# Performance work log

Measured on AMD Instinct MI355X. Metric: run time of the kernel, lower is better.

Reference implementation:

```python
import jax, jax.numpy as jnp
import numpy as np


def _dct_1d(x):
    # cat(x, flip(x)) -> fft(norm='forward') -> first L bins -> |.| * sign(Re)
    L = x.shape[-1]
    arr = jnp.concatenate([x, jnp.flip(x, axis=-1)], axis=-1)  # [..., 2L]
    f = jnp.fft.fft(arr, norm='forward')[..., :L]
    return jnp.abs(f) * jnp.sign(f.real)


def _dct_2d(x):
    row = _dct_1d(x)
    col = _dct_1d(row.swapaxes(-1, -2))
    return col.swapaxes(-1, -2)


def setup_inputs() -> dict:
    key = jax.random.key(0)
    k1, k2, k3 = jax.random.split(key, 3)
    B, C, H, W = 16, 256, 64, 64
    r = 16
    ip = jax.random.normal(k1, (B, C, H, W), dtype=jnp.float32)
    w1 = jax.random.normal(k2, (C, C // r), dtype=jnp.float32) * (1.0 / np.sqrt(C))
    w2 = jax.random.normal(k3, (C // r, C), dtype=jnp.float32) * (1.0 / np.sqrt(C // r))
    return {"ip": ip, "w1": w1, "w2": w2}


def reference(ip, w1, w2):
    B, C, H, W = ip.shape
    dct = _dct_2d(ip)                                  # [B,C,H,W]
    top1 = jnp.max(dct.reshape(B, C, H * W), axis=-1)  # top-k(k=1) == max, [B,C]
    h = jax.nn.relu(top1 @ w1)                         # [B, C//r]
    weights = jax.nn.sigmoid(h @ w2)                   # [B, C]
    return ip * weights[:, :, None, None]
```

## Files before the change

kernel.cpp:

```cpp
#include <hip/hip_runtime.h>
#include <math.h>


#define S 72

typedef __attribute__((ext_vector_type(8))) short bf16x8;
typedef __attribute__((ext_vector_type(4))) float f32x4;

__device__ inline unsigned short f2bf(float x) {
    union { float f; unsigned u; } v; v.f = x;
    unsigned r = v.u + 0x7FFF + ((v.u >> 16) & 1);
    return (unsigned short)(r >> 16);
}

__global__ __launch_bounds__(256, 4) void dct_max_kernel(const float* __restrict__ ip,
                                                         float* __restrict__ top1) {
    __shared__ unsigned short Dbf[64 * S];
    __shared__ unsigned short Xbf[64 * S];
    __shared__ unsigned short Tbf[64 * S];
    __shared__ float red[4];

    const int t = threadIdx.x;

#pragma unroll
    for (int i = 0; i < 16; ++i) {
        int idx = i * 256 + t;
        int u = idx >> 6, h = idx & 63;
        int mm = (u * (2 * h + 1)) & 255;
        Dbf[u * S + h] = f2bf(cospif((float)mm * (1.0f / 128.0f)));
    }

    const int wv = t >> 6;
    const int l = t & 63;
    const int m = l & 15;
    const int q = l >> 4;
    const int arow = (16 * wv + m) * S + 8 * q;
    const int xh = t >> 4;
    const int xw0 = (4 * t) & 63;

    const int bc0 = blockIdx.x * 4;
    const float4* src4 = (const float4*)(ip + (size_t)bc0 * 4096);

    float4 xv[4];
#pragma unroll
    for (int i = 0; i < 4; ++i) xv[i] = src4[i * 256 + t];

    __syncthreads();
    const bf16x8 da0 = *(const bf16x8*)&Dbf[arow];
    const bf16x8 da1 = *(const bf16x8*)&Dbf[arow + 32];

    for (int s = 0; s < 4; ++s) {
#pragma unroll
        for (int i = 0; i < 4; ++i) {
            ushort4 p;
            p.x = f2bf(xv[i].x); p.y = f2bf(xv[i].y);
            p.z = f2bf(xv[i].z); p.w = f2bf(xv[i].w);
            *(ushort4*)&Xbf[(16 * i + xh) * S + xw0] = p;
        }
        __syncthreads();

        if (s < 3) {
            const float4* nsrc = src4 + (size_t)(s + 1) * 1024;
#pragma unroll
            for (int i = 0; i < 4; ++i) xv[i] = nsrc[i * 256 + t];
        }

        f32x4 acc[4];
#pragma unroll
        for (int tn = 0; tn < 4; ++tn) {
            const int brow = (16 * tn + m) * S + 8 * q;
            bf16x8 b0 = *(const bf16x8*)&Xbf[brow];
            bf16x8 b1 = *(const bf16x8*)&Xbf[brow + 32];
            f32x4 c = {0.0f, 0.0f, 0.0f, 0.0f};
            c = __builtin_amdgcn_mfma_f32_16x16x32_bf16(da0, b0, c, 0, 0, 0);
            c = __builtin_amdgcn_mfma_f32_16x16x32_bf16(da1, b1, c, 0, 0, 0);
            acc[tn] = c;
        }
#pragma unroll
        for (int tn = 0; tn < 4; ++tn)
#pragma unroll
            for (int reg = 0; reg < 4; ++reg)
                Tbf[(16 * wv + 4 * q + reg) * S + 16 * tn + m] = f2bf(acc[tn][reg]);
        __syncthreads();

        bf16x8 ta0 = *(const bf16x8*)&Tbf[arow];
        bf16x8 ta1 = *(const bf16x8*)&Tbf[arow + 32];
        float mx = -3.4e38f;
#pragma unroll
        for (int tn = 0; tn < 4; ++tn) {
            const int brow = (16 * tn + m) * S + 8 * q;
            bf16x8 b0 = *(const bf16x8*)&Dbf[brow];
            bf16x8 b1 = *(const bf16x8*)&Dbf[brow + 32];
            f32x4 c = {0.0f, 0.0f, 0.0f, 0.0f};
            c = __builtin_amdgcn_mfma_f32_16x16x32_bf16(ta0, b0, c, 0, 0, 0);
            c = __builtin_amdgcn_mfma_f32_16x16x32_bf16(ta1, b1, c, 0, 0, 0);
            mx = fmaxf(mx, fmaxf(fmaxf(c[0], c[1]), fmaxf(c[2], c[3])));
        }

#pragma unroll
        for (int off = 32; off > 0; off >>= 1) mx = fmaxf(mx, __shfl_down(mx, off, 64));
        if (l == 0) red[wv] = mx;
        __syncthreads();
        if (t == 0) {
            float M = fmaxf(fmaxf(red[0], red[1]), fmaxf(red[2], red[3]));
            top1[bc0 + s] = M * (1.0f / 4096.0f);
        }
    }
}

__global__ __launch_bounds__(256, 4) void scale_kernel(const float* __restrict__ ip,
                                                       const float* __restrict__ top1,
                                                       const float* __restrict__ w1,
                                                       const float* __restrict__ w2,
                                                       float* __restrict__ out) {
    __shared__ float h_s[16];
    __shared__ float w_s[4];
    const int t = threadIdx.x;
    const int bc0 = blockIdx.x * 4;
    const int b = bc0 >> 8, c0 = bc0 & 255;

    const f32x4* ip4 = (const f32x4*)ip + (size_t)bc0 * 1024;
    f32x4* out4 = (f32x4*)out + (size_t)bc0 * 1024;

    const int j = t >> 4, i = t & 15;
    float tvals[16], wvals[16];
#pragma unroll
    for (int k = 0; k < 16; ++k) {
        int cc = i + 16 * k;
        tvals[k] = top1[b * 256 + cc];
        wvals[k] = w1[cc * 16 + j];
    }
    f32x4 v[16];
#pragma unroll
    for (int s = 0; s < 4; ++s)
#pragma unroll
        for (int k = 0; k < 4; ++k) v[s * 4 + k] = ip4[(size_t)s * 1024 + k * 256 + t];

    float partial = 0.0f;
#pragma unroll
    for (int k = 0; k < 16; ++k) partial = fmaf(tvals[k], wvals[k], partial);
#pragma unroll
    for (int off = 8; off > 0; off >>= 1) partial += __shfl_xor(partial, off, 16);
    if (i == 0) h_s[j] = fmaxf(partial, 0.0f);
    __syncthreads();

    if (t < 64) {
        const int sc = t >> 4, jj = t & 15;
        float p2 = h_s[jj] * w2[jj * 256 + (c0 + sc)];
#pragma unroll
        for (int off = 8; off > 0; off >>= 1) p2 += __shfl_xor(p2, off, 16);
        if (jj == 0) w_s[sc] = 1.0f / (1.0f + __expf(-p2));
    }
    __syncthreads();

#pragma unroll
    for (int s = 0; s < 4; ++s) {
        const float wt = w_s[s];
#pragma unroll
        for (int k = 0; k < 4; ++k) {
            f32x4 r = v[s * 4 + k] * wt;
            __builtin_nontemporal_store(r, &out4[(size_t)s * 1024 + k * 256 + t]);
        }
    }
}

extern "C" void kernel_launch(void* const* d_in, const int* in_sizes, int n_in,
                              void* d_out, int out_size, void* d_ws, size_t ws_size,
                              hipStream_t stream) {
    const float* ip = (const float*)d_in[0];
    const float* w1 = (const float*)d_in[1];
    const float* w2 = (const float*)d_in[2];
    float* out = (float*)d_out;
    float* top1 = (float*)d_ws;

    dct_max_kernel<<<1024, 256, 0, stream>>>(ip, top1);
    scale_kernel<<<1024, 256, 0, stream>>>(ip, top1, w1, w2, out);
}
```

Measured before the change: 127.1 us.

## Process one channel per block and use packed bf16 conversion instructions

Both kernels now handle one (batch, channel) plane per block instead of four, so the grid grows from 1024 to 4096 blocks and the per-block loop with register prefetch of the next plane goes away. The scale kernel keeps only four vectors in registers instead of sixteen, which lowers register pressure. Float-to-bf16 conversion now uses the hardware v_cvt_pk_bf16_f32 instruction instead of manual rounding. In exchange, each block rebuilds the DCT basis table in shared memory and recomputes the small MLP four times as often, and the software prefetch overlap is lost.

```diff
diff --git a/kernel.cpp b/kernel.cpp
--- a/kernel.cpp
+++ b/kernel.cpp
@@ -6,6 +6,12 @@
 
 typedef __attribute__((ext_vector_type(8))) short bf16x8;
 typedef __attribute__((ext_vector_type(4))) float f32x4;
+
+__device__ inline unsigned cvt_pk_bf16(float lo, float hi) {
+    unsigned r;
+    asm("v_cvt_pk_bf16_f32 %0, %1, %2" : "=v"(r) : "v"(lo), "v"(hi));
+    return r;
+}
 
 __device__ inline unsigned short f2bf(float x) {
     union { float f; unsigned u; } v; v.f = x;
@@ -21,6 +27,12 @@
     __shared__ float red[4];
 
     const int t = threadIdx.x;
+    const int bc = blockIdx.x;
+
+    const float4* src4 = (const float4*)(ip + (size_t)bc * 4096);
+    float4 xv[4];
+#pragma unroll
+    for (int i = 0; i < 4; ++i) xv[i] = src4[i * 256 + t];
 
 #pragma unroll
     for (int i = 0; i < 16; ++i) {
@@ -38,73 +50,58 @@
     const int xh = t >> 4;
     const int xw0 = (4 * t) & 63;
 
-    const int bc0 = blockIdx.x * 4;
-    const float4* src4 = (const float4*)(ip + (size_t)bc0 * 4096);
+#pragma unroll
+    for (int i = 0; i < 4; ++i) {
+        uint2 p;
+        p.x = cvt_pk_bf16(xv[i].x, xv[i].y);
+        p.y = cvt_pk_bf16(xv[i].z, xv[i].w);
+        *(uint2*)&Xbf[(16 * i + xh) * S + xw0] = p;
+    }
+    __syncthreads();
 
-    float4 xv[4];
-#pragma unroll
-    for (int i = 0; i < 4; ++i) xv[i] = src4[i * 256 + t];
-
-    __syncthreads();
     const bf16x8 da0 = *(const bf16x8*)&Dbf[arow];
     const bf16x8 da1 = *(const bf16x8*)&Dbf[arow + 32];
 
-    for (int s = 0; s < 4; ++s) {
+    f32x4 acc[4];
 #pragma unroll
-        for (int i = 0; i < 4; ++i) {
-            ushort4 p;
-            p.x = f2bf(xv[i].x); p.y = f2bf(xv[i].y);
-            p.z = f2bf(xv[i].z); p.w = f2bf(xv[i].w);
-            *(ushort4*)&Xbf[(16 * i + xh) * S + xw0] = p;
-        }
-        __syncthreads();
+    for (int tn = 0; tn < 4; ++tn) {
+        const int brow = (16 * tn + m) * S + 8 * q;
+        bf16x8 b0 = *(const bf16x8*)&Xbf[brow];
+        bf16x8 b1 = *(const bf16x8*)&Xbf[brow + 32];
+        f32x4 c = {0.0f, 0.0f, 0.0f, 0.0f};
+        c = __builtin_amdgcn_mfma_f32_16x16x32_bf16(da0, b0, c, 0, 0, 0);
+        c = __builtin_amdgcn_mfma_f32_16x16x32_bf16(da1, b1, c, 0, 0, 0);
+        acc[tn] = c;
+    }
+#pragma unroll
+    for (int tn = 0; tn < 4; ++tn)
+#pragma unroll
+        for (int reg = 0; reg < 4; ++reg)
+            Tbf[(16 * wv + 4 * q + reg) * S + 16 * tn + m] =
+                (unsigned short)cvt_pk_bf16(acc[tn][reg], acc[tn][reg]);
+    __syncthreads();
 
-        if (s < 3) {
-            const float4* nsrc = src4 + (size_t)(s + 1) * 1024;
+    bf16x8 ta0 = *(const bf16x8*)&Tbf[arow];
+    bf16x8 ta1 = *(const bf16x8*)&Tbf[arow + 32];
+    float mx = -3.4e38f;
 #pragma unroll
-            for (int i = 0; i < 4; ++i) xv[i] = nsrc[i * 256 + t];
-        }
-
-        f32x4 acc[4];
-#pragma unroll
-        for (int tn = 0; tn < 4; ++tn) {
-            const int brow = (16 * tn + m) * S + 8 * q;
-            bf16x8 b0 = *(const bf16x8*)&Xbf[brow];
-            bf16x8 b1 = *(const bf16x8*)&Xbf[brow + 32];
-            f32x4 c = {0.0f, 0.0f, 0.0f, 0.0f};
-            c = __builtin_amdgcn_mfma_f32_16x16x32_bf16(da0, b0, c, 0, 0, 0);
-            c = __builtin_amdgcn_mfma_f32_16x16x32_bf16(da1, b1, c, 0, 0, 0);
-            acc[tn] = c;
-        }
-#pragma unroll
-        for (int tn = 0; tn < 4; ++tn)
-#pragma unroll
-            for (int reg = 0; reg < 4; ++reg)
-                Tbf[(16 * wv + 4 * q + reg) * S + 16 * tn + m] = f2bf(acc[tn][reg]);
-        __syncthreads();
-
-        bf16x8 ta0 = *(const bf16x8*)&Tbf[arow];
-        bf16x8 ta1 = *(const bf16x8*)&Tbf[arow + 32];
-        float mx = -3.4e38f;
-#pragma unroll
-        for (int tn = 0; tn < 4; ++tn) {
-            const int brow = (16 * tn + m) * S + 8 * q;
-            bf16x8 b0 = *(const bf16x8*)&Dbf[brow];
-            bf16x8 b1 = *(const bf16x8*)&Dbf[brow + 32];
-            f32x4 c = {0.0f, 0.0f, 0.0f, 0.0f};
-            c = __builtin_amdgcn_mfma_f32_16x16x32_bf16(ta0, b0, c, 0, 0, 0);
-            c = __builtin_amdgcn_mfma_f32_16x16x32_bf16(ta1, b1, c, 0, 0, 0);
-            mx = fmaxf(mx, fmaxf(fmaxf(c[0], c[1]), fmaxf(c[2], c[3])));
-        }
+    for (int tn = 0; tn < 4; ++tn) {
+        const int brow = (16 * tn + m) * S + 8 * q;
+        bf16x8 b0 = *(const bf16x8*)&Dbf[brow];
+        bf16x8 b1 = *(const bf16x8*)&Dbf[brow + 32];
+        f32x4 c = {0.0f, 0.0f, 0.0f, 0.0f};
+        c = __builtin_amdgcn_mfma_f32_16x16x32_bf16(ta0, b0, c, 0, 0, 0);
+        c = __builtin_amdgcn_mfma_f32_16x16x32_bf16(ta1, b1, c, 0, 0, 0);
+        mx = fmaxf(mx, fmaxf(fmaxf(c[0], c[1]), fmaxf(c[2], c[3])));
+    }
 
 #pragma unroll
-        for (int off = 32; off > 0; off >>= 1) mx = fmaxf(mx, __shfl_down(mx, off, 64));
-        if (l == 0) red[wv] = mx;
-        __syncthreads();
-        if (t == 0) {
-            float M = fmaxf(fmaxf(red[0], red[1]), fmaxf(red[2], red[3]));
-            top1[bc0 + s] = M * (1.0f / 4096.0f);
-        }
+    for (int off = 32; off > 0; off >>= 1) mx = fmaxf(mx, __shfl_down(mx, off, 64));
+    if (l == 0) red[wv] = mx;
+    __syncthreads();
+    if (t == 0) {
+        float M = fmaxf(fmaxf(red[0], red[1]), fmaxf(red[2], red[3]));
+        top1[bc] = M * (1.0f / 4096.0f);
     }
 }
 
@@ -114,54 +111,42 @@
                                                        const float* __restrict__ w2,
                                                        float* __restrict__ out) {
     __shared__ float h_s[16];
-    __shared__ float w_s[4];
+    __shared__ float wsc;
     const int t = threadIdx.x;
-    const int bc0 = blockIdx.x * 4;
-    const int b = bc0 >> 8, c0 = bc0 & 255;
+    const int bc = blockIdx.x;
+    const int b = bc >> 8, c = bc & 255;
 
-    const f32x4* ip4 = (const f32x4*)ip + (size_t)bc0 * 1024;
-    f32x4* out4 = (f32x4*)out + (size_t)bc0 * 1024;
+    const f32x4* ip4 = (const f32x4*)ip + (size_t)bc * 1024;
+    f32x4* out4 = (f32x4*)out + (size_t)bc * 1024;
+
+    f32x4 v[4];
+#pragma unroll
+    for (int k = 0; k < 4; ++k) v[k] = ip4[k * 256 + t];
 
     const int j = t >> 4, i = t & 15;
-    float tvals[16], wvals[16];
+    float partial = 0.0f;
 #pragma unroll
     for (int k = 0; k < 16; ++k) {
         int cc = i + 16 * k;
-        tvals[k] = top1[b * 256 + cc];
-        wvals[k] = w1[cc * 16 + j];
+        partial = fmaf(top1[b * 256 + cc], w1[cc * 16 + j], partial);
     }
-    f32x4 v[16];
-#pragma unroll
-    for (int s = 0; s < 4; ++s)
-#pragma unroll
-        for (int k = 0; k < 4; ++k) v[s * 4 + k] = ip4[(size_t)s * 1024 + k * 256 + t];
-
-    float partial = 0.0f;
-#pragma unroll
-    for (int k = 0; k < 16; ++k) partial = fmaf(tvals[k], wvals[k], partial);
 #pragma unroll
     for (int off = 8; off > 0; off >>= 1) partial += __shfl_xor(partial, off, 16);
     if (i == 0) h_s[j] = fmaxf(partial, 0.0f);
     __syncthreads();
 
-    if (t < 64) {
-        const int sc = t >> 4, jj = t & 15;
-        float p2 = h_s[jj] * w2[jj * 256 + (c0 + sc)];
+    if (t < 16) {
+        float p2 = h_s[t] * w2[t * 256 + c];
 #pragma unroll
         for (int off = 8; off > 0; off >>= 1) p2 += __shfl_xor(p2, off, 16);
-        if (jj == 0) w_s[sc] = 1.0f / (1.0f + __expf(-p2));
+        if (t == 0) wsc = 1.0f / (1.0f + __expf(-p2));
     }
     __syncthreads();
 
+    const float wt = wsc;
 #pragma unroll
-    for (int s = 0; s < 4; ++s) {
-        const float wt = w_s[s];
-#pragma unroll
-        for (int k = 0; k < 4; ++k) {
-            f32x4 r = v[s * 4 + k] * wt;
-            __builtin_nontemporal_store(r, &out4[(size_t)s * 1024 + k * 256 + t]);
-        }
-    }
+    for (int k = 0; k < 4; ++k)
+        __builtin_nontemporal_store(v[k] * wt, &out4[k * 256 + t]);
 }
 
 extern "C" void kernel_launch(void* const* d_in, const int* in_sizes, int n_in,
@@ -173,6 +158,6 @@
     float* out = (float*)d_out;
     float* top1 = (float*)d_ws;
 
-    dct_max_kernel<<<1024, 256, 0, stream>>>(ip, top1);
-    scale_kernel<<<1024, 256, 0, stream>>>(ip, top1, w1, w2, out);
+    dct_max_kernel<<<4096, 256, 0, stream>>>(ip, top1);
+    scale_kernel<<<4096, 256, 0, stream>>>(ip, top1, w1, w2, out);
 }
```

Result: slower. 144.9 us (+14.0%).
